# Optimization experiments

Measured on AMD Instinct MI355X. Metric: run time of the kernel, lower is better.

## Reference

```python
import jax, jax.numpy as jnp
import numpy as np

B, T, I, H = 32, 8192, 1, 256
OS_FACTOR = 1.5  # delay_near=1, delay_far=2, alpha=0.5, allpass coeff=(1-a)/(1+a)=1/3


def setup_inputs() -> dict:
    key = jax.random.key(0)
    ks = jax.random.split(key, 5)
    s = 1.0 / np.sqrt(H)  # torch LSTMCell init scale
    x = jax.random.normal(ks[0], (B, T, I), jnp.float32)
    W_ih = jax.random.normal(ks[1], (4 * H, I), jnp.float32) * s
    W_hh = jax.random.normal(ks[2], (4 * H, H), jnp.float32) * s
    b_ih = jax.random.normal(ks[3], (4 * H,), jnp.float32) * s
    b_hh = jax.random.normal(ks[4], (4 * H,), jnp.float32) * s
    return {"x": x, "W_ih": W_ih, "W_hh": W_hh, "b_ih": b_ih, "b_hh": b_hh}


def reference(x, W_ih, W_hh, b_ih, b_hh):
    # APDL_RNN forward with LSTMCell, h=None, os_factor=1.5.
    delay_near = int(np.floor(OS_FACTOR))          # 1
    alpha = OS_FACTOR - delay_near                 # 0.5
    coeff = (1.0 - alpha) / (1.0 + alpha)          # 1/3
    Bsz = x.shape[0]
    Hh = W_hh.shape[1]
    S = 2 * Hh  # LSTM state = concat(h, c)

    # Precompute input projection for all timesteps: [B, T, 4H]
    xg = jnp.einsum('bti,gi->btg', x, W_ih) + b_ih

    zero = jnp.zeros((Bsz, S), x.dtype)
    # carry: (state[i-1], state[i-2], ap_state) -- zero-init matches h=None
    init = (zero, zero, zero)

    def step(carry, xg_t):
        s1, s2, ap = carry
        # first-order allpass interpolated delayed state
        ap = coeff * (s1 - ap) + s2
        h, c = ap[:, :Hh], ap[:, Hh:]
        gates = xg_t + h @ W_hh.T + b_hh  # [B, 4H]
        i_g, f_g, g_g, o_g = jnp.split(gates, 4, axis=-1)  # torch gate order
        c_new = jax.nn.sigmoid(f_g) * c + jax.nn.sigmoid(i_g) * jnp.tanh(g_g)
        h_new = jax.nn.sigmoid(o_g) * jnp.tanh(c_new)
        s_new = jnp.concatenate([h_new, c_new], axis=-1)
        return (s_new, s1, ap), s_new

    (_, _, ap_final), states = jax.lax.scan(step, init, jnp.swapaxes(xg, 0, 1))
    states = jnp.swapaxes(states, 0, 1)  # [B, T, 2H]
    y = states[..., :Hh]
    return y, states[..., :Hh], states[..., Hh:], ap_final
```

## Files before the change

kernel.cpp:

```cpp
#include <hip/hip_runtime.h>


#define Bn 32
#define Tn 8192
#define Hn 256
#define HPAD 136

typedef float floatx4 __attribute__((ext_vector_type(4)));

static constexpr float kCoeff = 1.0f / 3.0f;

__device__ __forceinline__ float sigf(float x) {
  return __builtin_amdgcn_rcpf(1.0f + __expf(-x));
}
__device__ __forceinline__ float tanhf_fast(float x) {
  return 1.0f - 2.0f * __builtin_amdgcn_rcpf(1.0f + __expf(2.0f * x));
}
__device__ __forceinline__ float pick4(int d, float v0, float v1, float v2, float v3) {
  float r = (d == 0) ? v0 : v1;
  r = (d == 2) ? v2 : r;
  r = (d == 3) ? v3 : r;
  return r;
}
__device__ __forceinline__ unsigned tagf(float v, unsigned tg) {
  return ((__float_as_uint(v) + 256u) & ~511u) | tg;
}

__global__ void init_ws(unsigned int* ws) {
  int i = blockIdx.x * 256 + threadIdx.x;
  if (i < 16384) ws[i] = 0;
}

#define LOADW(i) floatx4 w##i = *(const floatx4*)(wrow + 4 * (i))
#define PINW(i) asm volatile("" : "+v"(w##i))
#define ACC8(i, j, K)                                           \
  {                                                             \
    floatx4 p = *(const floatx4*)&hsp[(K)];                     \
    floatx4 q = *(const floatx4*)&hsp[(K) + 4];                 \
    a0 = fmaf(w##i[0], p[0], a0); a1 = fmaf(w##i[1], p[1], a1); \
    a2 = fmaf(w##i[2], p[2], a2); a3 = fmaf(w##i[3], p[3], a3); \
    a4 = fmaf(w##j[0], q[0], a4); a5 = fmaf(w##j[1], q[1], a5); \
    a6 = fmaf(w##j[2], q[2], a6); a7 = fmaf(w##j[3], q[3], a7); \
  }

__global__ __launch_bounds__(512, 2) void apdl_rnn(
    const float* __restrict__ x, const float* __restrict__ W_ih,
    const float* __restrict__ W_hh, const float* __restrict__ b_ih,
    const float* __restrict__ b_hh, float* __restrict__ out,
    unsigned long long* __restrict__ pub) {
  const int bid = blockIdx.x;
  const int w = bid >> 5;
  const int b = bid & 31;
  const int tid = (int)threadIdx.x;
  const int hf = tid & 1;
  const int p = tid >> 1;
  const int g = p & 3;
  const int ul = p >> 2;
  const int u = w * 64 + ul;
  const int row = g * Hn + u;

  __shared__ __align__(16) float xs[Tn];
  __shared__ __align__(16) float hs2[2][2 * HPAD];

  for (int i = tid; i < Tn; i += 512) xs[i] = x[b * Tn + i];

  const float* wrow = W_hh + row * Hn + hf * 128;
  LOADW(0);  LOADW(1);  LOADW(2);  LOADW(3);  LOADW(4);  LOADW(5);  LOADW(6);  LOADW(7);
  LOADW(8);  LOADW(9);  LOADW(10); LOADW(11); LOADW(12); LOADW(13); LOADW(14); LOADW(15);
  LOADW(16); LOADW(17); LOADW(18); LOADW(19); LOADW(20); LOADW(21); LOADW(22); LOADW(23);
  LOADW(24); LOADW(25); LOADW(26); LOADW(27); LOADW(28); LOADW(29); LOADW(30); LOADW(31);
  asm volatile("s_waitcnt vmcnt(0)" ::: "memory");
  PINW(0);  PINW(1);  PINW(2);  PINW(3);  PINW(4);  PINW(5);  PINW(6);  PINW(7);
  PINW(8);  PINW(9);  PINW(10); PINW(11); PINW(12); PINW(13); PINW(14); PINW(15);
  PINW(16); PINW(17); PINW(18); PINW(19); PINW(20); PINW(21); PINW(22); PINW(23);
  PINW(24); PINW(25); PINW(26); PINW(27); PINW(28); PINW(29); PINW(30); PINW(31);

  const float wih = W_ih[row];
  const float bias = b_ih[row] + b_hh[row];

  unsigned long long* mypub = pub + b * 2 * 128;

  const bool poller = (tid < 96);
  const int slot = poller ? (tid < w * 32 ? tid : tid + 32) : 0;

  float s1_h = 0.f, s1_c = 0.f, ap_h = 0.f, ap_c = 0.f;

  for (int t = 0; t < Tn; ++t) {
    if (t == 0) {
      if (tid < Hn) hs2[0][tid + ((tid >> 7) << 3)] = 0.f;
    } else if (poller) {
      const unsigned long long* pa = mypub + (t & 1) * 128 + slot;
      const unsigned tg = (unsigned)t & 511u;
      unsigned long long pk;
      unsigned lo, hi;
      do {
        pk = __hip_atomic_load(pa, __ATOMIC_RELAXED, __HIP_MEMORY_SCOPE_AGENT);
        lo = (unsigned)pk; hi = (unsigned)(pk >> 32);
      } while (((lo ^ tg) & 511u) | ((hi ^ tg) & 511u));
      const int u0 = 2 * slot;
      const int idx0 = u0 + ((u0 >> 7) << 3);
      *(float2*)&hs2[t & 1][idx0] =
          make_float2(__uint_as_float(lo), __uint_as_float(hi));
    }
    __syncthreads();

    const float* hsp = &hs2[t & 1][hf * HPAD];
    float a0 = 0.f, a1 = 0.f, a2 = 0.f, a3 = 0.f;
    float a4 = 0.f, a5 = 0.f, a6 = 0.f, a7 = 0.f;
    ACC8(0, 1, 0);     ACC8(2, 3, 8);     ACC8(4, 5, 16);    ACC8(6, 7, 24);
    ACC8(8, 9, 32);    ACC8(10, 11, 40);  ACC8(12, 13, 48);  ACC8(14, 15, 56);
    ACC8(16, 17, 64);  ACC8(18, 19, 72);  ACC8(20, 21, 80);  ACC8(22, 23, 88);
    ACC8(24, 25, 96);  ACC8(26, 27, 104); ACC8(28, 29, 112); ACC8(30, 31, 120);
    float half = ((a0 + a1) + (a2 + a3)) + ((a4 + a5) + (a6 + a7));
    float dot = half + __shfl_xor(half, 1);
    float raw = dot + xs[t] * wih + bias;

    float act = (g == 2) ? tanhf_fast(raw) : sigf(raw);
    float v1 = __shfl_xor(act, 2);
    float v2 = __shfl_xor(act, 4);
    float v3 = __shfl_xor(act, 6);
    float ai = pick4(g,     act, v1, v2, v3);
    float af = pick4(g ^ 1, act, v1, v2, v3);
    float ag = pick4(g ^ 2, act, v1, v2, v3);
    float ao = pick4(g ^ 3, act, v1, v2, v3);

    float c_new = af * ap_c + ai * ag;
    float h_new = ao * tanhf_fast(c_new);

    if (t < Tn - 1) {
      float nh = kCoeff * (h_new - ap_h) + s1_h;
      if (g == 3 && hf == 0) {
        unsigned vb = tagf(nh, (unsigned)(t + 1) & 511u);
        unsigned pb = __shfl_xor(vb, 8);
        if ((tid & 15) == 6) {
          const int s = w * 32 + (tid >> 4);
          unsigned long long pk = (unsigned long long)vb |
                                  ((unsigned long long)pb << 32);
          __hip_atomic_store(mypub + ((t + 1) & 1) * 128 + s, pk, __ATOMIC_RELAXED,
                             __HIP_MEMORY_SCOPE_AGENT);
          const int u0 = 2 * s;
          const int idx0 = u0 + ((u0 >> 7) << 3);
          *(float2*)&hs2[(t + 1) & 1][idx0] =
              make_float2(__uint_as_float(vb), __uint_as_float(pb));
        }
      }
      float nc = kCoeff * (c_new - ap_c) + s1_c;
      s1_h = h_new; s1_c = c_new; ap_h = nh; ap_c = nc;
    } else {
      if (g == 0 && hf == 0)      out[201326592 + b * 512 + u] = ap_h;
      else if (g == 1 && hf == 0) out[201326592 + b * 512 + 256 + u] = ap_c;
    }

    int o = (b * Tn + t) * Hn + u;
    if (hf == 0) {
      if (g == 0)      out[o] = h_new;
      else if (g == 2) out[67108864 + o] = h_new;
      else if (g == 1) out[134217728 + o] = c_new;
    }
  }
}

extern "C" void kernel_launch(void* const* d_in, const int* in_sizes, int n_in,
                              void* d_out, int out_size, void* d_ws, size_t ws_size,
                              hipStream_t stream) {
  const float* x = (const float*)d_in[0];
  const float* W_ih = (const float*)d_in[1];
  const float* W_hh = (const float*)d_in[2];
  const float* b_ih = (const float*)d_in[3];
  const float* b_hh = (const float*)d_in[4];
  float* out = (float*)d_out;
  unsigned long long* pub = (unsigned long long*)d_ws;

  init_ws<<<64, 256, 0, stream>>>((unsigned int*)d_ws);
  apdl_rnn<<<128, 512, 0, stream>>>(x, W_ih, W_hh, b_ih, b_hh, out, pub);
}
```

Before: 10.76 ms.

## Add redundant secondary pollers with LDS done-flags and use atomic exchange for publish

Each remote h-slot is now polled by two waves, a primary and a staggered secondary that sleeps briefly first. Whichever sees the tagged value first writes it to LDS and sets a shared done flag so the other exits early. The aim is to cut the tail latency of the cross-block spin-wait on every timestep. The publish store becomes an atomic exchange, presumably to push it out to L2 sooner. The cost is extra polling traffic, LDS flag reads inside the spin loop, and a possible race if a stale done value matches t.

Measured after the change: 12.82 ms. 19.1% more time.

```diff
diff --git a/kernel.cpp b/kernel.cpp
--- a/kernel.cpp
+++ b/kernel.cpp
@@ -24,6 +24,24 @@
 }
 __device__ __forceinline__ unsigned tagf(float v, unsigned tg) {
   return ((__float_as_uint(v) + 256u) & ~511u) | tg;
+}
+
+__device__ __forceinline__ void poll_stage(const unsigned long long* pa, int* dn,
+                                           float* dst, unsigned tg, int t) {
+  for (;;) {
+    unsigned long long pk =
+        __hip_atomic_load(pa, __ATOMIC_RELAXED, __HIP_MEMORY_SCOPE_AGENT);
+    unsigned lo = (unsigned)pk, hi = (unsigned)(pk >> 32);
+    if (!(((lo ^ tg) & 511u) | ((hi ^ tg) & 511u))) {
+      *(float2*)dst = make_float2(__uint_as_float(lo), __uint_as_float(hi));
+      asm volatile("s_waitcnt lgkmcnt(0)" ::: "memory");
+      __hip_atomic_store(dn, t, __ATOMIC_RELAXED,
+                         __HIP_MEMORY_SCOPE_WORKGROUP);
+      return;
+    }
+    if (__hip_atomic_load(dn, __ATOMIC_RELAXED, __HIP_MEMORY_SCOPE_WORKGROUP) == t)
+      return;
+  }
 }
 
 __global__ void init_ws(unsigned int* ws) {
@@ -61,8 +79,10 @@
 
   __shared__ __align__(16) float xs[Tn];
   __shared__ __align__(16) float hs2[2][2 * HPAD];
+  __shared__ int done[96];
 
   for (int i = tid; i < Tn; i += 512) xs[i] = x[b * Tn + i];
+  if (tid < 96) done[tid] = 0;
 
   const float* wrow = W_hh + row * Hn + hf * 128;
   LOADW(0);  LOADW(1);  LOADW(2);  LOADW(3);  LOADW(4);  LOADW(5);  LOADW(6);  LOADW(7);
@@ -80,27 +100,24 @@
 
   unsigned long long* mypub = pub + b * 2 * 128;
 
-  const bool poller = (tid < 96);
-  const int slot = poller ? (tid < w * 32 ? tid : tid + 32) : 0;
+  const bool prim = (tid < 96);
+  const bool secd = (tid >= 128 && tid < 224);
+  const int pi = prim ? tid : (secd ? tid - 128 : 0);
+  const int slot = (pi < w * 32) ? pi : pi + 32;
 
   float s1_h = 0.f, s1_c = 0.f, ap_h = 0.f, ap_c = 0.f;
 
   for (int t = 0; t < Tn; ++t) {
     if (t == 0) {
-      if (tid < Hn) hs2[0][tid + ((tid >> 7) << 3)] = 0.f;
-    } else if (poller) {
-      const unsigned long long* pa = mypub + (t & 1) * 128 + slot;
-      const unsigned tg = (unsigned)t & 511u;
-      unsigned long long pk;
-      unsigned lo, hi;
-      do {
-        pk = __hip_atomic_load(pa, __ATOMIC_RELAXED, __HIP_MEMORY_SCOPE_AGENT);
-        lo = (unsigned)pk; hi = (unsigned)(pk >> 32);
-      } while (((lo ^ tg) & 511u) | ((hi ^ tg) & 511u));
-      const int u0 = 2 * slot;
-      const int idx0 = u0 + ((u0 >> 7) << 3);
-      *(float2*)&hs2[t & 1][idx0] =
-          make_float2(__uint_as_float(lo), __uint_as_float(hi));
+      if (tid < 128) {
+        const int u0 = 2 * tid, idx0 = u0 + ((u0 >> 7) << 3);
+        *(float2*)&hs2[0][idx0] = make_float2(0.f, 0.f);
+      }
+    } else if (prim || secd) {
+      if (secd) __builtin_amdgcn_s_sleep(5);
+      const int u0 = 2 * slot, idx0 = u0 + ((u0 >> 7) << 3);
+      poll_stage(mypub + (t & 1) * 128 + slot, &done[pi], &hs2[t & 1][idx0],
+                 (unsigned)t & 511u, t);
     }
     __syncthreads();
 
@@ -136,8 +153,8 @@
           const int s = w * 32 + (tid >> 4);
           unsigned long long pk = (unsigned long long)vb |
                                   ((unsigned long long)pb << 32);
-          __hip_atomic_store(mypub + ((t + 1) & 1) * 128 + s, pk, __ATOMIC_RELAXED,
-                             __HIP_MEMORY_SCOPE_AGENT);
+          __hip_atomic_exchange(mypub + ((t + 1) & 1) * 128 + s, pk,
+                                __ATOMIC_RELAXED, __HIP_MEMORY_SCOPE_AGENT);
           const int u0 = 2 * s;
           const int idx0 = u0 + ((u0 >> 7) << 3);
           *(float2*)&hs2[(t + 1) & 1][idx0] =
```

## Split hidden units across eight blocks per batch with quarter-row dot products

Applied to the files above, without the earlier changes.

The 256 hidden units are now split across 8 blocks per batch instead of 4, so the grid goes from 128 to 256 blocks. Each thread keeps a quarter of a W_hh row (64 weights) in registers instead of half, and the dot product is finished with two cross-lane shuffle reductions. This halves the per-thread FMA chain on the serial timestep critical path and spreads the work over more compute units. In exchange, each block must poll more published state slots from other blocks every step (112 pollers instead of 96), which adds cross-block synchronisation cost.

After: 9.188 ms, median of 2. 14.6% less time.

```diff
diff --git a/kernel.cpp b/kernel.cpp
--- a/kernel.cpp
+++ b/kernel.cpp
@@ -4,7 +4,7 @@
 #define Bn 32
 #define Tn 8192
 #define Hn 256
-#define HPAD 136
+#define QP 72
 
 typedef float floatx4 __attribute__((ext_vector_type(4)));
 
@@ -25,6 +25,7 @@
 __device__ __forceinline__ unsigned tagf(float v, unsigned tg) {
   return ((__float_as_uint(v) + 256u) & ~511u) | tg;
 }
+__device__ __forceinline__ int pidx(int u) { return u + ((u >> 6) << 3); }
 
 __global__ void init_ws(unsigned int* ws) {
   int i = blockIdx.x * 256 + threadIdx.x;
@@ -52,42 +53,40 @@
   const int w = bid >> 5;
   const int b = bid & 31;
   const int tid = (int)threadIdx.x;
-  const int hf = tid & 1;
-  const int p = tid >> 1;
-  const int g = p & 3;
-  const int ul = p >> 2;
-  const int u = w * 64 + ul;
+  const int q = tid & 3;
+  const int r = tid >> 2;
+  const int g = r & 3;
+  const int ul = r >> 2;
+  const int u = w * 32 + ul;
   const int row = g * Hn + u;
 
   __shared__ __align__(16) float xs[Tn];
-  __shared__ __align__(16) float hs2[2][2 * HPAD];
+  __shared__ __align__(16) float hs2[2][4 * QP];
 
   for (int i = tid; i < Tn; i += 512) xs[i] = x[b * Tn + i];
 
-  const float* wrow = W_hh + row * Hn + hf * 128;
+  const float* wrow = W_hh + row * Hn + q * 64;
   LOADW(0);  LOADW(1);  LOADW(2);  LOADW(3);  LOADW(4);  LOADW(5);  LOADW(6);  LOADW(7);
   LOADW(8);  LOADW(9);  LOADW(10); LOADW(11); LOADW(12); LOADW(13); LOADW(14); LOADW(15);
-  LOADW(16); LOADW(17); LOADW(18); LOADW(19); LOADW(20); LOADW(21); LOADW(22); LOADW(23);
-  LOADW(24); LOADW(25); LOADW(26); LOADW(27); LOADW(28); LOADW(29); LOADW(30); LOADW(31);
   asm volatile("s_waitcnt vmcnt(0)" ::: "memory");
   PINW(0);  PINW(1);  PINW(2);  PINW(3);  PINW(4);  PINW(5);  PINW(6);  PINW(7);
   PINW(8);  PINW(9);  PINW(10); PINW(11); PINW(12); PINW(13); PINW(14); PINW(15);
-  PINW(16); PINW(17); PINW(18); PINW(19); PINW(20); PINW(21); PINW(22); PINW(23);
-  PINW(24); PINW(25); PINW(26); PINW(27); PINW(28); PINW(29); PINW(30); PINW(31);
 
   const float wih = W_ih[row];
   const float bias = b_ih[row] + b_hh[row];
 
   unsigned long long* mypub = pub + b * 2 * 128;
 
-  const bool poller = (tid < 96);
-  const int slot = poller ? (tid < w * 32 ? tid : tid + 32) : 0;
+  const bool poller = (tid < 112);
+  const int slot = poller ? (tid < w * 16 ? tid : tid + 16) : 0;
 
   float s1_h = 0.f, s1_c = 0.f, ap_h = 0.f, ap_c = 0.f;
 
   for (int t = 0; t < Tn; ++t) {
     if (t == 0) {
-      if (tid < Hn) hs2[0][tid + ((tid >> 7) << 3)] = 0.f;
+      if (tid < 128) {
+        *(float2*)&hs2[0][pidx(2 * tid)] = make_float2(0.f, 0.f);
+      }
     } else if (poller) {
       const unsigned long long* pa = mypub + (t & 1) * 128 + slot;
       const unsigned tg = (unsigned)t & 511u;
@@ -97,28 +96,25 @@
         pk = __hip_atomic_load(pa, __ATOMIC_RELAXED, __HIP_MEMORY_SCOPE_AGENT);
         lo = (unsigned)pk; hi = (unsigned)(pk >> 32);
       } while (((lo ^ tg) & 511u) | ((hi ^ tg) & 511u));
-      const int u0 = 2 * slot;
-      const int idx0 = u0 + ((u0 >> 7) << 3);
-      *(float2*)&hs2[t & 1][idx0] =
+      *(float2*)&hs2[t & 1][pidx(2 * slot)] =
           make_float2(__uint_as_float(lo), __uint_as_float(hi));
     }
     __syncthreads();
 
-    const float* hsp = &hs2[t & 1][hf * HPAD];
+    const float* hsp = &hs2[t & 1][q * QP];
     float a0 = 0.f, a1 = 0.f, a2 = 0.f, a3 = 0.f;
     float a4 = 0.f, a5 = 0.f, a6 = 0.f, a7 = 0.f;
-    ACC8(0, 1, 0);     ACC8(2, 3, 8);     ACC8(4, 5, 16);    ACC8(6, 7, 24);
-    ACC8(8, 9, 32);    ACC8(10, 11, 40);  ACC8(12, 13, 48);  ACC8(14, 15, 56);
-    ACC8(16, 17, 64);  ACC8(18, 19, 72);  ACC8(20, 21, 80);  ACC8(22, 23, 88);
-    ACC8(24, 25, 96);  ACC8(26, 27, 104); ACC8(28, 29, 112); ACC8(30, 31, 120);
-    float half = ((a0 + a1) + (a2 + a3)) + ((a4 + a5) + (a6 + a7));
-    float dot = half + __shfl_xor(half, 1);
+    ACC8(0, 1, 0);   ACC8(2, 3, 8);   ACC8(4, 5, 16);  ACC8(6, 7, 24);
+    ACC8(8, 9, 32);  ACC8(10, 11, 40); ACC8(12, 13, 48); ACC8(14, 15, 56);
+    float qd = ((a0 + a1) + (a2 + a3)) + ((a4 + a5) + (a6 + a7));
+    float d0 = qd + __shfl_xor(qd, 1);
+    float dot = d0 + __shfl_xor(d0, 2);
     float raw = dot + xs[t] * wih + bias;
 
     float act = (g == 2) ? tanhf_fast(raw) : sigf(raw);
-    float v1 = __shfl_xor(act, 2);
-    float v2 = __shfl_xor(act, 4);
-    float v3 = __shfl_xor(act, 6);
+    float v1 = __shfl_xor(act, 4);
+    float v2 = __shfl_xor(act, 8);
+    float v3 = __shfl_xor(act, 12);
     float ai = pick4(g,     act, v1, v2, v3);
     float af = pick4(g ^ 1, act, v1, v2, v3);
     float ag = pick4(g ^ 2, act, v1, v2, v3);
@@ -129,30 +125,26 @@
 
     if (t < Tn - 1) {
       float nh = kCoeff * (h_new - ap_h) + s1_h;
-      if (g == 3 && hf == 0) {
-        unsigned vb = tagf(nh, (unsigned)(t + 1) & 511u);
-        unsigned pb = __shfl_xor(vb, 8);
-        if ((tid & 15) == 6) {
-          const int s = w * 32 + (tid >> 4);
-          unsigned long long pk = (unsigned long long)vb |
-                                  ((unsigned long long)pb << 32);
-          __hip_atomic_store(mypub + ((t + 1) & 1) * 128 + s, pk, __ATOMIC_RELAXED,
-                             __HIP_MEMORY_SCOPE_AGENT);
-          const int u0 = 2 * s;
-          const int idx0 = u0 + ((u0 >> 7) << 3);
-          *(float2*)&hs2[(t + 1) & 1][idx0] =
-              make_float2(__uint_as_float(vb), __uint_as_float(pb));
-        }
+      unsigned vb = tagf(nh, (unsigned)(t + 1) & 511u);
+      unsigned pb = __shfl_xor(vb, 16);
+      if ((tid & 31) == 12) {
+        const int s = w * 16 + (tid >> 5);
+        unsigned long long pk = (unsigned long long)vb |
+                                ((unsigned long long)pb << 32);
+        __hip_atomic_store(mypub + ((t + 1) & 1) * 128 + s, pk, __ATOMIC_RELAXED,
+                           __HIP_MEMORY_SCOPE_AGENT);
+        *(float2*)&hs2[(t + 1) & 1][pidx(2 * s)] =
+            make_float2(__uint_as_float(vb), __uint_as_float(pb));
       }
       float nc = kCoeff * (c_new - ap_c) + s1_c;
       s1_h = h_new; s1_c = c_new; ap_h = nh; ap_c = nc;
     } else {
-      if (g == 0 && hf == 0)      out[201326592 + b * 512 + u] = ap_h;
-      else if (g == 1 && hf == 0) out[201326592 + b * 512 + 256 + u] = ap_c;
+      if (g == 0 && q == 0)      out[201326592 + b * 512 + u] = ap_h;
+      else if (g == 1 && q == 0) out[201326592 + b * 512 + 256 + u] = ap_c;
     }
 
     int o = (b * Tn + t) * Hn + u;
-    if (hf == 0) {
+    if (q == 0) {
       if (g == 0)      out[o] = h_new;
       else if (g == 2) out[67108864 + o] = h_new;
       else if (g == 1) out[134217728 + o] = c_new;
@@ -172,5 +164,5 @@
   unsigned long long* pub = (unsigned long long*)d_ws;
 
   init_ws<<<64, 256, 0, stream>>>((unsigned int*)d_ws);
-  apdl_rnn<<<128, 512, 0, stream>>>(x, W_ih, W_hh, b_ih, b_hh, out, pub);
+  apdl_rnn<<<256, 512, 0, stream>>>(x, W_ih, W_hh, b_ih, b_hh, out, pub);
 }
```
